# Performance work log

Hardware: AMD Instinct MI355X
Metric: run time of the kernel (lower is better)

Reference implementation:

```python
import jax, jax.numpy as jnp
import numpy as np

# ---- HashGridPlanesEncoder config (hybrid-k-planes) ----
NUM_LEVELS = 16
LEVEL_DIM = 2
BASE_RES = 16
DESIRED_RES = 2048
LOG2_HASHMAP = 19
D = 2  # grid_nd: each plane encoder is a 2D hash grid
N_PTS = 1048576
COO_COMBS = [(0, 1), (0, 2), (1, 2)]
HASH_PRIME_1 = 2654435761  # torch-ngp fast_hash prime for dim 1 (dim 0 prime is 1)


def _level_constants():
    # Mirrors torch-ngp GridEncoder offset/resolution computation.
    pls = 2.0 ** (np.log2(DESIRED_RES / BASE_RES) / (NUM_LEVELS - 1))
    max_params = 2 ** LOG2_HASHMAP
    scales, res, sizes, offs = [], [], [], [0]
    for l in range(NUM_LEVELS):
        s = BASE_RES * pls ** l - 1.0          # kernel: scale = exp2(l*S + H) - 1
        r = int(np.ceil(s)) + 1                # kernel: resolution = ceil(scale) + 1
        p = min(max_params, (r + 1) ** D)      # align_corners=False -> (res+1)^D
        p = int(np.ceil(p / 8) * 8)            # round up to multiple of 8
        scales.append(s); res.append(r); sizes.append(p); offs.append(offs[-1] + p)
    return (np.array(scales, np.float32), np.array(res, np.int64),
            np.array(sizes, np.int64), np.array(offs[:-1], np.int64), offs[-1])


SCALES, RES, SIZES, OFFSETS, TOTAL_PARAMS = _level_constants()
USE_HASH = ((RES + 1) ** D) > SIZES  # static per-level: dense linear index vs spatial hash


def _encode_plane(x2, table):
    """x2: [N,2] coords in [0,1]; table: [TOTAL_PARAMS, LEVEL_DIM]. Returns [N, L*C]."""
    n = x2.shape[0]
    scales = jnp.asarray(SCALES)
    pos = x2[:, None, :] * scales[None, :, None] + 0.5           # [N,L,2] (align_corners=False)
    pg_f = jnp.floor(pos)
    frac = pos - pg_f                                            # [N,L,2]
    pg = pg_f.astype(jnp.uint32)
    corners = jnp.array([[0, 0], [1, 0], [0, 1], [1, 1]], jnp.uint32)  # [4,2]
    cpos = pg[:, :, None, :] + corners[None, None]               # [N,L,4,2]
    cmask = corners.astype(bool)[None, None]                     # [1,1,4,2]
    w = jnp.where(cmask, frac[:, :, None, :], 1.0 - frac[:, :, None, :]).prod(-1)  # [N,L,4]
    stride1 = jnp.asarray((RES + 1).astype(np.uint32))           # [L]
    linear = cpos[..., 0] + cpos[..., 1] * stride1[None, :, None]
    hashed = cpos[..., 0] ^ (cpos[..., 1] * jnp.uint32(HASH_PRIME_1))  # uint32 wrap-around
    idx = jnp.where(jnp.asarray(USE_HASH)[None, :, None], hashed, linear)
    idx = idx % jnp.asarray(SIZES.astype(np.uint32))[None, :, None]
    idx = (idx + jnp.asarray(OFFSETS.astype(np.uint32))[None, :, None]).astype(jnp.int32)
    feats = table[idx]                                           # [N,L,4,C] gather
    out = (w[..., None] * feats).sum(axis=2)                     # [N,L,C] bilinear interp
    return out.reshape(n, NUM_LEVELS * LEVEL_DIM)


def setup_inputs() -> dict:
    key = jax.random.key(0)
    kp, k0, k1, k2 = jax.random.split(key, 4)
    pts = jax.random.uniform(kp, (N_PTS, 3), dtype=jnp.float32)  # coords (treated as in [-1,1] domain)
    std = 1e-4  # GridEncoder init: embeddings.uniform_(-1e-4, 1e-4)
    mk = lambda k: jax.random.uniform(k, (TOTAL_PARAMS, LEVEL_DIM), jnp.float32, -std, std)
    return {"pts": pts, "table_xy": mk(k0), "table_xz": mk(k1), "table_yz": mk(k2)}


def reference(pts, table_xy, table_xz, table_yz):
    # GridEncoder.forward normalizes inputs: (x + bound) / (2*bound), bound=1
    u = (pts + 1.0) * 0.5
    tables = (table_xy, table_xz, table_yz)
    out = _encode_plane(u[:, list(COO_COMBS[0])], tables[0])
    for comb, tab in zip(COO_COMBS[1:], tables[1:]):
        out = out + _encode_plane(u[:, list(comb)], tab)
    return out
```

## Files before the change

### kernel.cpp

```cpp
#include <hip/hip_runtime.h>
#include <hip/hip_fp16.h>
#include <cmath>

#define NLEV 16
#define HASH_START 12
#define HMASK ((1u << 19) - 1u)
#define HASH_PRIME 2654435761u
#define LDS_WORDS 14160

typedef float    f4 __attribute__((ext_vector_type(4)));
typedef unsigned u4 __attribute__((ext_vector_type(4)));

struct LvlC {
  float scale[NLEV];
  unsigned stride[NLEV];
  unsigned offset[NLEV];
};

__device__ __forceinline__ float2 h2f(unsigned u) {
  return __half22float2(__builtin_bit_cast(__half2, u));
}
__device__ __forceinline__ void nt_store4(float* p, float a, float b, float c, float d) {
  f4 v = {a, b, c, d};
  __builtin_nontemporal_store(v, reinterpret_cast<f4*>(p));
}

__global__ __launch_bounds__(256) void k_convert(
    const float2* __restrict__ t0, const float2* __restrict__ t1,
    const float2* __restrict__ t2, unsigned* __restrict__ dst, unsigned total)
{
  unsigned g = blockIdx.x * 256 + threadIdx.x;
  unsigned stp = gridDim.x * 256;
  unsigned tot3 = 3u * total;
  for (unsigned e = g; e < tot3; e += stp) {
    const float2* src; unsigned i = e;
    if (i < total)            { src = t0; }
    else if (i < 2u * total)  { src = t1; i -= total; }
    else                      { src = t2; i -= 2u * total; }
    float2 v = src[i];
    __half2 h = __floats2half2_rn(v.x, v.y);
    __builtin_nontemporal_store(__builtin_bit_cast(unsigned, h), dst + e);
  }
}

__global__ __launch_bounds__(256) void k_dense1011(
    const float* __restrict__ pts, const unsigned* __restrict__ tab,
    unsigned* __restrict__ s10, unsigned* __restrict__ s11,
    LvlC lc, unsigned total, int half)
{
  int t = blockIdx.x * 256 + threadIdx.x;
  if (t >= half) return;
  const int idx[2] = {t, t + half};

  float ua[2][3], ub[2][3];
#pragma unroll
  for (int k = 0; k < 2; ++k) {
    float u0 = (pts[3 * idx[k] + 0] + 1.f) * .5f;
    float u1 = (pts[3 * idx[k] + 1] + 1.f) * .5f;
    float u2 = (pts[3 * idx[k] + 2] + 1.f) * .5f;
    ua[k][0] = u0; ub[k][0] = u1;
    ua[k][1] = u0; ub[k][1] = u2;
    ua[k][2] = u1; ub[k][2] = u2;
  }

  uint2 g[2][2][3][2];
  float rx[2][2][3], ry[2][2][3];
#pragma unroll
  for (int k = 0; k < 2; ++k)
#pragma unroll
    for (int l = 0; l < 2; ++l) {
      const float sc = lc.scale[10 + l];
      const unsigned st = lc.stride[10 + l], o = lc.offset[10 + l];
#pragma unroll
      for (int p = 0; p < 3; ++p) {
        float px = ua[k][p] * sc + .5f, py = ub[k][p] * sc + .5f;
        float fx = floorf(px), fy = floorf(py);
        rx[k][l][p] = px - fx; ry[k][l][p] = py - fy;
        unsigned i00 = (unsigned)fx + (unsigned)fy * st + o;
        const unsigned* tp = tab + (size_t)p * total;
        g[k][l][p][0] = *reinterpret_cast<const uint2*>(tp + i00);
        g[k][l][p][1] = *reinterpret_cast<const uint2*>(tp + i00 + st);
      }
    }

#pragma unroll
  for (int k = 0; k < 2; ++k)
#pragma unroll
    for (int l = 0; l < 2; ++l) {
      float s0 = 0.f, s1 = 0.f;
#pragma unroll
      for (int p = 0; p < 3; ++p) {
        float x = rx[k][l][p], y = ry[k][l][p];
        float w00 = (1.f - x) * (1.f - y), w10 = x * (1.f - y);
        float w01 = (1.f - x) * y,          w11 = x * y;
        float2 f00 = h2f(g[k][l][p][0].x), f10 = h2f(g[k][l][p][0].y);
        float2 f01 = h2f(g[k][l][p][1].x), f11 = h2f(g[k][l][p][1].y);
        s0 += w00 * f00.x + w10 * f10.x + w01 * f01.x + w11 * f11.x;
        s1 += w00 * f00.y + w10 * f10.y + w01 * f01.y + w11 * f11.y;
      }
      unsigned hv = __builtin_bit_cast(unsigned, __floats2half2_rn(s0, s1));
      unsigned* sl = l ? s11 : s10;
      __builtin_nontemporal_store(hv, sl + idx[k]);
    }
}

__device__ __forceinline__ void hash_row(
    const unsigned* __restrict__ tp, unsigned x0, unsigned hy,
    unsigned& g0, unsigned& g1)
{
  unsigned a0 = (x0 ^ hy) & HMASK;
  if ((x0 & 1u) == 0u) {
    uint2 v = *reinterpret_cast<const uint2*>(tp + (a0 & ~1u));
    bool hi = (a0 & 1u) != 0u;
    g0 = hi ? v.y : v.x;
    g1 = hi ? v.x : v.y;
  } else {
    g0 = tp[a0];
    g1 = tp[((x0 + 1u) ^ hy) & HMASK];
  }
}

__global__ __launch_bounds__(256) void k_hash_lvl(
    const float* __restrict__ pts, const unsigned* __restrict__ tab,
    unsigned* __restrict__ slice, float sc, unsigned o, unsigned total, int half)
{
  int t = blockIdx.x * 256 + threadIdx.x;
  if (t >= half) return;
  const int idx[2] = {t, t + half};

  float ua[2][3], ub[2][3];
#pragma unroll
  for (int k = 0; k < 2; ++k) {
    float u0 = (pts[3 * idx[k] + 0] + 1.f) * .5f;
    float u1 = (pts[3 * idx[k] + 1] + 1.f) * .5f;
    float u2 = (pts[3 * idx[k] + 2] + 1.f) * .5f;
    ua[k][0] = u0; ub[k][0] = u1;
    ua[k][1] = u0; ub[k][1] = u2;
    ua[k][2] = u1; ub[k][2] = u2;
  }

  unsigned g[2][3][4];
  float rx[2][3], ry[2][3];
#pragma unroll
  for (int k = 0; k < 2; ++k)
#pragma unroll
    for (int p = 0; p < 3; ++p) {
      float px = ua[k][p] * sc + .5f, py = ub[k][p] * sc + .5f;
      float fx = floorf(px), fy = floorf(py);
      rx[k][p] = px - fx; ry[k][p] = py - fy;
      unsigned x0 = (unsigned)fx, y0 = (unsigned)fy;
      unsigned hy0 = y0 * HASH_PRIME, hy1 = hy0 + HASH_PRIME;
      const unsigned* tp = tab + (size_t)p * total + o;
      hash_row(tp, x0, hy0, g[k][p][0], g[k][p][1]);
      hash_row(tp, x0, hy1, g[k][p][2], g[k][p][3]);
    }

#pragma unroll
  for (int k = 0; k < 2; ++k) {
    float s0 = 0.f, s1 = 0.f;
#pragma unroll
    for (int p = 0; p < 3; ++p) {
      float x = rx[k][p], y = ry[k][p];
      float w00 = (1.f - x) * (1.f - y), w10 = x * (1.f - y);
      float w01 = (1.f - x) * y,          w11 = x * y;
      float2 f00 = h2f(g[k][p][0]), f10 = h2f(g[k][p][1]);
      float2 f01 = h2f(g[k][p][2]), f11 = h2f(g[k][p][3]);
      s0 += w00 * f00.x + w10 * f10.x + w01 * f01.x + w11 * f11.x;
      s1 += w00 * f00.y + w10 * f10.y + w01 * f01.y + w11 * f11.y;
    }
    __builtin_nontemporal_store(
        __builtin_bit_cast(unsigned, __floats2half2_rn(s0, s1)), slice + idx[k]);
  }
}

__global__ __launch_bounds__(512) void k_final(
    const float* __restrict__ pts, const unsigned* __restrict__ tab,
    const unsigned* __restrict__ slices,
    float* __restrict__ out, LvlC lc, unsigned total, int n)
{
  __shared__ unsigned lds[LDS_WORDS];
  int i = blockIdx.x * 512 + threadIdx.x;

  float u0 = (pts[3 * i + 0] + 1.f) * .5f;
  float u1 = (pts[3 * i + 1] + 1.f) * .5f;
  float u2 = (pts[3 * i + 2] + 1.f) * .5f;
  const float ua[3] = {u0, u0, u1}, ub[3] = {u1, u2, u2};

  float res[12];
#pragma unroll
  for (int j = 0; j < 12; ++j) res[j] = 0.f;

  for (int p = 0; p < 3; ++p) {
    if (p) __syncthreads();
    const u4* src = reinterpret_cast<const u4*>(tab + (size_t)p * total);
    for (unsigned e = threadIdx.x; e < LDS_WORDS / 4; e += 512)
      reinterpret_cast<u4*>(lds)[e] = src[e];
    __syncthreads();
#pragma unroll
    for (int l = 0; l < 6; ++l) {
      float px = ua[p] * lc.scale[l] + .5f, py = ub[p] * lc.scale[l] + .5f;
      float fx = floorf(px), fy = floorf(py);
      float x = px - fx, y = py - fy;
      unsigned st = lc.stride[l];
      unsigned i00 = (unsigned)fx + (unsigned)fy * st + lc.offset[l];
      float2 f00 = h2f(lds[i00]),      f10 = h2f(lds[i00 + 1]);
      float2 f01 = h2f(lds[i00 + st]), f11 = h2f(lds[i00 + st + 1]);
      float w00 = (1.f - x) * (1.f - y), w10 = x * (1.f - y);
      float w01 = (1.f - x) * y,          w11 = x * y;
      res[2 * l + 0] += w00 * f00.x + w10 * f10.x + w01 * f01.x + w11 * f11.x;
      res[2 * l + 1] += w00 * f00.y + w10 * f10.y + w01 * f01.y + w11 * f11.y;
    }
  }

  float res69[8];
#pragma unroll
  for (int grp = 0; grp < 2; ++grp) {
    uint2 g[2][3][2];
    float gx[2][3], gy[2][3];
#pragma unroll
    for (int h = 0; h < 2; ++h) {
      const int l = 6 + 2 * grp + h;
      const float sc = lc.scale[l];
      const unsigned st = lc.stride[l], o = lc.offset[l];
#pragma unroll
      for (int p = 0; p < 3; ++p) {
        float px = ua[p] * sc + .5f, py = ub[p] * sc + .5f;
        float fx = floorf(px), fy = floorf(py);
        gx[h][p] = px - fx; gy[h][p] = py - fy;
        unsigned i00 = (unsigned)fx + (unsigned)fy * st + o;
        const unsigned* tp = tab + (size_t)p * total;
        g[h][p][0] = *reinterpret_cast<const uint2*>(tp + i00);
        g[h][p][1] = *reinterpret_cast<const uint2*>(tp + i00 + st);
      }
    }
#pragma unroll
    for (int h = 0; h < 2; ++h) {
      float s0 = 0.f, s1 = 0.f;
#pragma unroll
      for (int p = 0; p < 3; ++p) {
        float x = gx[h][p], y = gy[h][p];
        float w00 = (1.f - x) * (1.f - y), w10 = x * (1.f - y);
        float w01 = (1.f - x) * y,          w11 = x * y;
        float2 f00 = h2f(g[h][p][0].x), f10 = h2f(g[h][p][0].y);
        float2 f01 = h2f(g[h][p][1].x), f11 = h2f(g[h][p][1].y);
        s0 += w00 * f00.x + w10 * f10.x + w01 * f01.x + w11 * f11.x;
        s1 += w00 * f00.y + w10 * f10.y + w01 * f01.y + w11 * f11.y;
      }
      res69[4 * grp + 2 * h + 0] = s0;
      res69[4 * grp + 2 * h + 1] = s1;
    }
  }

  unsigned sl[6];
#pragma unroll
  for (int j = 0; j < 6; ++j) sl[j] = slices[(size_t)j * n + i];

  float v[32];
#pragma unroll
  for (int j = 0; j < 12; ++j) v[j] = res[j];
#pragma unroll
  for (int j = 0; j < 8; ++j) v[12 + j] = res69[j];
#pragma unroll
  for (int j = 0; j < 6; ++j) {
    float2 f = h2f(sl[j]);
    v[20 + 2 * j] = f.x; v[20 + 2 * j + 1] = f.y;
  }
  float* orow = out + (size_t)i * 32;
#pragma unroll
  for (int j = 0; j < 8; ++j)
    nt_store4(orow + 4 * j, v[4 * j], v[4 * j + 1], v[4 * j + 2], v[4 * j + 3]);
}

__global__ __launch_bounds__(256) void k_fallback(
    const float* __restrict__ pts, const float2* __restrict__ txy,
    const float2* __restrict__ txz, const float2* __restrict__ tyz,
    float* __restrict__ out, LvlC lc, int n)
{
  int i = blockIdx.x * 256 + threadIdx.x;
  if (i >= n) return;
  float u0 = (pts[3 * i + 0] + 1.f) * .5f;
  float u1 = (pts[3 * i + 1] + 1.f) * .5f;
  float u2 = (pts[3 * i + 2] + 1.f) * .5f;
  const float ua[3] = {u0, u0, u1}, ub[3] = {u1, u2, u2};
  const float2* tabs[3] = {txy, txz, tyz};
  float acc[32];
#pragma unroll
  for (int j = 0; j < 32; ++j) acc[j] = 0.f;
#pragma unroll
  for (int l = 0; l < NLEV; ++l) {
    const float sc = lc.scale[l];
    const unsigned o = lc.offset[l], s = lc.stride[l];
#pragma unroll
    for (int p = 0; p < 3; ++p) {
      const float2* t = tabs[p];
      float px = ua[p] * sc + .5f, py = ub[p] * sc + .5f;
      float fx = floorf(px), fy = floorf(py);
      float rx = px - fx, ry = py - fy;
      unsigned x0 = (unsigned)fx, y0 = (unsigned)fy;
      float w00 = (1.f - rx) * (1.f - ry), w10 = rx * (1.f - ry);
      float w01 = (1.f - rx) * ry,          w11 = rx * ry;
      float2 f00, f10, f01, f11;
      if (l >= HASH_START) {
        unsigned hy0 = y0 * HASH_PRIME, hy1 = hy0 + HASH_PRIME;
        f00 = t[o + ((x0 ^ hy0) & HMASK)];
        f10 = t[o + (((x0 + 1u) ^ hy0) & HMASK)];
        f01 = t[o + ((x0 ^ hy1) & HMASK)];
        f11 = t[o + (((x0 + 1u) ^ hy1) & HMASK)];
      } else {
        unsigned i00 = x0 + y0 * s;
        float4 r0 = *reinterpret_cast<const float4*>(t + o + i00);
        float4 r1 = *reinterpret_cast<const float4*>(t + o + i00 + s);
        f00 = make_float2(r0.x, r0.y); f10 = make_float2(r0.z, r0.w);
        f01 = make_float2(r1.x, r1.y); f11 = make_float2(r1.z, r1.w);
      }
      acc[2 * l + 0] += w00 * f00.x + w10 * f10.x + w01 * f01.x + w11 * f11.x;
      acc[2 * l + 1] += w00 * f00.y + w10 * f10.y + w01 * f01.y + w11 * f11.y;
    }
  }
  float* orow = out + (size_t)i * 32;
#pragma unroll
  for (int j = 0; j < 8; ++j)
    nt_store4(orow + 4 * j, acc[4 * j], acc[4 * j + 1], acc[4 * j + 2], acc[4 * j + 3]);
}

static unsigned compute_levels(LvlC* lc)
{
  const double pls = std::pow(2.0, std::log2(2048.0 / 16.0) / 15.0);
  unsigned long long off = 0;
  for (int l = 0; l < NLEV; ++l) {
    double s = 16.0 * std::pow(pls, (double)l) - 1.0;
    lc->scale[l] = (float)s;
    long long r = (long long)std::ceil(s) + 1;
    long long dense = (r + 1) * (r + 1);
    long long sz = dense < (1LL << 19) ? dense : (1LL << 19);
    sz = ((sz + 7) / 8) * 8;
    lc->stride[l] = (unsigned)(r + 1);
    lc->offset[l] = (unsigned)off;
    off += (unsigned long long)sz;
  }
  return (unsigned)off;
}

extern "C" void kernel_launch(void* const* d_in, const int* in_sizes, int n_in,
                              void* d_out, int out_size, void* d_ws, size_t ws_size,
                              hipStream_t stream) {
  const float*  pts = (const float*)d_in[0];
  const float2* txy = (const float2*)d_in[1];
  const float2* txz = (const float2*)d_in[2];
  const float2* tyz = (const float2*)d_in[3];
  float* out = (float*)d_out;
  int n = in_sizes[0] / 3;

  LvlC lc;
  unsigned total = compute_levels(&lc);

  size_t tab_bytes = (size_t)3 * total * 4;
  size_t tab_al = (tab_bytes + 255) & ~(size_t)255;
  size_t need = tab_al + (size_t)6 * n * 4;

  bool ok = (n % 512 == 0) && (lc.offset[6] == LDS_WORDS) && (ws_size >= need);
  for (int l = HASH_START; l < NLEV; ++l) {
    unsigned sz = ((l + 1 < NLEV) ? lc.offset[l + 1] : total) - lc.offset[l];
    ok = ok && (sz == (1u << 19));
  }

  int block = 256;
  int grid = (n + block - 1) / block;
  if (!ok) {
    k_fallback<<<grid, block, 0, stream>>>(pts, txy, txz, tyz, out, lc, n);
    return;
  }

  unsigned* tab16 = (unsigned*)d_ws;
  unsigned* slices = (unsigned*)((char*)d_ws + tab_al);

  int half = n / 2;
  int gridh = half / block;

  k_convert<<<2048, 256, 0, stream>>>(txy, txz, tyz, tab16, total);
  k_dense1011<<<gridh, block, 0, stream>>>(pts, tab16, slices, slices + (size_t)n,
                                           lc, total, half);
  for (int l = HASH_START; l < NLEV; ++l)
    k_hash_lvl<<<gridh, block, 0, stream>>>(pts, tab16, slices + (size_t)(l - 10) * n,
                                            lc.scale[l], lc.offset[l], total, half);
  k_final<<<n / 512, 512, 0, stream>>>(pts, tab16, slices, out, lc, total, n);
}
```

Before: 366.3 us.

## Halve LDS footprint by staging level 5 separately; hoist slice loads; use plain stores

The LDS table for k_final shrinks from 14160 words to 7432: levels 0-4 are staged first, then level 5 is loaded separately into the same buffer, which adds an extra load and syncs per plane. The smaller LDS use is meant to let more workgroups share a CU and hide latency better. The slice loads move to the top of the kernel so their global latency overlaps the compute. Output stores change from nontemporal to ordinary float4 stores, which may alter cache behaviour on the large output write.

```diff
diff --git a/kernel.cpp b/kernel.cpp
--- a/kernel.cpp
+++ b/kernel.cpp
@@ -6,7 +6,8 @@
 #define HASH_START 12
 #define HMASK ((1u << 19) - 1u)
 #define HASH_PRIME 2654435761u
-#define LDS_WORDS 14160
+#define LDSA_WORDS 7432
+#define LDS5_WORDS 6728
 
 typedef float    f4 __attribute__((ext_vector_type(4)));
 typedef unsigned u4 __attribute__((ext_vector_type(4)));
@@ -178,8 +179,12 @@
     const unsigned* __restrict__ slices,
     float* __restrict__ out, LvlC lc, unsigned total, int n)
 {
-  __shared__ unsigned lds[LDS_WORDS];
+  __shared__ unsigned lds[LDSA_WORDS];
   int i = blockIdx.x * 512 + threadIdx.x;
+
+  unsigned sl[6];
+#pragma unroll
+  for (int j = 0; j < 6; ++j) sl[j] = slices[(size_t)j * n + i];
 
   float u0 = (pts[3 * i + 0] + 1.f) * .5f;
   float u1 = (pts[3 * i + 1] + 1.f) * .5f;
@@ -191,13 +196,13 @@
   for (int j = 0; j < 12; ++j) res[j] = 0.f;
 
   for (int p = 0; p < 3; ++p) {
+    const unsigned* tp = tab + (size_t)p * total;
     if (p) __syncthreads();
-    const u4* src = reinterpret_cast<const u4*>(tab + (size_t)p * total);
-    for (unsigned e = threadIdx.x; e < LDS_WORDS / 4; e += 512)
-      reinterpret_cast<u4*>(lds)[e] = src[e];
+    for (unsigned e = threadIdx.x; e < LDSA_WORDS / 4; e += 512)
+      reinterpret_cast<u4*>(lds)[e] = reinterpret_cast<const u4*>(tp)[e];
     __syncthreads();
 #pragma unroll
-    for (int l = 0; l < 6; ++l) {
+    for (int l = 0; l < 5; ++l) {
       float px = ua[p] * lc.scale[l] + .5f, py = ub[p] * lc.scale[l] + .5f;
       float fx = floorf(px), fy = floorf(py);
       float x = px - fx, y = py - fy;
@@ -210,6 +215,24 @@
       res[2 * l + 0] += w00 * f00.x + w10 * f10.x + w01 * f01.x + w11 * f11.x;
       res[2 * l + 1] += w00 * f00.y + w10 * f10.y + w01 * f01.y + w11 * f11.y;
     }
+    __syncthreads();
+    {
+      const u4* src5 = reinterpret_cast<const u4*>(tp + lc.offset[5]);
+      for (unsigned e = threadIdx.x; e < LDS5_WORDS / 4; e += 512)
+        reinterpret_cast<u4*>(lds)[e] = src5[e];
+      __syncthreads();
+      float px = ua[p] * lc.scale[5] + .5f, py = ub[p] * lc.scale[5] + .5f;
+      float fx = floorf(px), fy = floorf(py);
+      float x = px - fx, y = py - fy;
+      unsigned st = lc.stride[5];
+      unsigned i00 = (unsigned)fx + (unsigned)fy * st;
+      float2 f00 = h2f(lds[i00]),      f10 = h2f(lds[i00 + 1]);
+      float2 f01 = h2f(lds[i00 + st]), f11 = h2f(lds[i00 + st + 1]);
+      float w00 = (1.f - x) * (1.f - y), w10 = x * (1.f - y);
+      float w01 = (1.f - x) * y,          w11 = x * y;
+      res[10] += w00 * f00.x + w10 * f10.x + w01 * f01.x + w11 * f11.x;
+      res[11] += w00 * f00.y + w10 * f10.y + w01 * f01.y + w11 * f11.y;
+    }
   }
 
   float res69[8];
@@ -251,10 +274,6 @@
     }
   }
 
-  unsigned sl[6];
-#pragma unroll
-  for (int j = 0; j < 6; ++j) sl[j] = slices[(size_t)j * n + i];
-
   float v[32];
 #pragma unroll
   for (int j = 0; j < 12; ++j) v[j] = res[j];
@@ -265,10 +284,10 @@
     float2 f = h2f(sl[j]);
     v[20 + 2 * j] = f.x; v[20 + 2 * j + 1] = f.y;
   }
-  float* orow = out + (size_t)i * 32;
+  float4* o4 = (float4*)(out + (size_t)i * 32);
 #pragma unroll
   for (int j = 0; j < 8; ++j)
-    nt_store4(orow + 4 * j, v[4 * j], v[4 * j + 1], v[4 * j + 2], v[4 * j + 3]);
+    o4[j] = make_float4(v[4 * j], v[4 * j + 1], v[4 * j + 2], v[4 * j + 3]);
 }
 
 __global__ __launch_bounds__(256) void k_fallback(
@@ -317,10 +336,10 @@
       acc[2 * l + 1] += w00 * f00.y + w10 * f10.y + w01 * f01.y + w11 * f11.y;
     }
   }
-  float* orow = out + (size_t)i * 32;
+  float4* o4 = (float4*)(out + (size_t)i * 32);
 #pragma unroll
   for (int j = 0; j < 8; ++j)
-    nt_store4(orow + 4 * j, acc[4 * j], acc[4 * j + 1], acc[4 * j + 2], acc[4 * j + 3]);
+    o4[j] = make_float4(acc[4 * j], acc[4 * j + 1], acc[4 * j + 2], acc[4 * j + 3]);
 }
 
 static unsigned compute_levels(LvlC* lc)
@@ -358,7 +377,8 @@
   size_t tab_al = (tab_bytes + 255) & ~(size_t)255;
   size_t need = tab_al + (size_t)6 * n * 4;
 
-  bool ok = (n % 512 == 0) && (lc.offset[6] == LDS_WORDS) && (ws_size >= need);
+  bool ok = (n % 512 == 0) && (lc.offset[5] == LDSA_WORDS) &&
+            (lc.offset[6] - lc.offset[5] == LDS5_WORDS) && (ws_size >= need);
   for (int l = HASH_START; l < NLEV; ++l) {
     unsigned sz = ((l + 1 < NLEV) ? lc.offset[l + 1] : total) - lc.offset[l];
     ok = ok && (sz == (1u << 19));
```

After: 374.7 us. 1.02x slower.

## Move levels 6-9 out of final kernel into separate dense-pair slice passes

Applied to the files above, without the earlier changes.

Generalizes the dense level-pair kernel to take per-level constants and, when workspace allows, runs it for level pairs 6-7, 8-9 and 10-11, writing ten fp16 slices. The final kernel then only does the LDS levels 0-5 and unpacks slices, with the slice loads issued at kernel start. Output stores change from nontemporal to plain float4 stores. This shortens the final kernel's register-heavy gather phase at the cost of two extra launches and more slice traffic through memory.

```diff
diff --git a/kernel.cpp b/kernel.cpp
--- a/kernel.cpp
+++ b/kernel.cpp
@@ -19,10 +19,6 @@
 
 __device__ __forceinline__ float2 h2f(unsigned u) {
   return __half22float2(__builtin_bit_cast(__half2, u));
-}
-__device__ __forceinline__ void nt_store4(float* p, float a, float b, float c, float d) {
-  f4 v = {a, b, c, d};
-  __builtin_nontemporal_store(v, reinterpret_cast<f4*>(p));
 }
 
 __global__ __launch_bounds__(256) void k_convert(
@@ -43,10 +39,12 @@
   }
 }
 
-__global__ __launch_bounds__(256) void k_dense1011(
+__global__ __launch_bounds__(256) void k_dense_pair(
     const float* __restrict__ pts, const unsigned* __restrict__ tab,
-    unsigned* __restrict__ s10, unsigned* __restrict__ s11,
-    LvlC lc, unsigned total, int half)
+    unsigned* __restrict__ sA, unsigned* __restrict__ sB,
+    float scA, unsigned stA, unsigned oA,
+    float scB, unsigned stB, unsigned oB,
+    unsigned total, int half)
 {
   int t = blockIdx.x * 256 + threadIdx.x;
   if (t >= half) return;
@@ -62,26 +60,25 @@
     ua[k][1] = u0; ub[k][1] = u2;
     ua[k][2] = u1; ub[k][2] = u2;
   }
+  const float sc[2] = {scA, scB};
+  const unsigned st[2] = {stA, stB}, o[2] = {oA, oB};
 
   uint2 g[2][2][3][2];
   float rx[2][2][3], ry[2][2][3];
 #pragma unroll
   for (int k = 0; k < 2; ++k)
 #pragma unroll
-    for (int l = 0; l < 2; ++l) {
-      const float sc = lc.scale[10 + l];
-      const unsigned st = lc.stride[10 + l], o = lc.offset[10 + l];
+    for (int l = 0; l < 2; ++l)
 #pragma unroll
       for (int p = 0; p < 3; ++p) {
-        float px = ua[k][p] * sc + .5f, py = ub[k][p] * sc + .5f;
+        float px = ua[k][p] * sc[l] + .5f, py = ub[k][p] * sc[l] + .5f;
         float fx = floorf(px), fy = floorf(py);
         rx[k][l][p] = px - fx; ry[k][l][p] = py - fy;
-        unsigned i00 = (unsigned)fx + (unsigned)fy * st + o;
+        unsigned i00 = (unsigned)fx + (unsigned)fy * st[l] + o[l];
         const unsigned* tp = tab + (size_t)p * total;
         g[k][l][p][0] = *reinterpret_cast<const uint2*>(tp + i00);
-        g[k][l][p][1] = *reinterpret_cast<const uint2*>(tp + i00 + st);
+        g[k][l][p][1] = *reinterpret_cast<const uint2*>(tp + i00 + st[l]);
       }
-    }
 
 #pragma unroll
   for (int k = 0; k < 2; ++k)
@@ -99,8 +96,7 @@
         s1 += w00 * f00.y + w10 * f10.y + w01 * f01.y + w11 * f11.y;
       }
       unsigned hv = __builtin_bit_cast(unsigned, __floats2half2_rn(s0, s1));
-      unsigned* sl = l ? s11 : s10;
-      __builtin_nontemporal_store(hv, sl + idx[k]);
+      __builtin_nontemporal_store(hv, (l ? sB : sA) + idx[k]);
     }
 }
 
@@ -173,6 +169,7 @@
   }
 }
 
+template <bool DO69>
 __global__ __launch_bounds__(512) void k_final(
     const float* __restrict__ pts, const unsigned* __restrict__ tab,
     const unsigned* __restrict__ slices,
@@ -180,6 +177,11 @@
 {
   __shared__ unsigned lds[LDS_WORDS];
   int i = blockIdx.x * 512 + threadIdx.x;
+
+  const int NS = DO69 ? 6 : 10;
+  unsigned sl[DO69 ? 6 : 10];
+#pragma unroll
+  for (int j = 0; j < NS; ++j) sl[j] = slices[(size_t)j * n + i];
 
   float u0 = (pts[3 * i + 0] + 1.f) * .5f;
   float u1 = (pts[3 * i + 1] + 1.f) * .5f;
@@ -212,63 +214,65 @@
     }
   }
 
-  float res69[8];
-#pragma unroll
-  for (int grp = 0; grp < 2; ++grp) {
-    uint2 g[2][3][2];
-    float gx[2][3], gy[2][3];
-#pragma unroll
-    for (int h = 0; h < 2; ++h) {
-      const int l = 6 + 2 * grp + h;
-      const float sc = lc.scale[l];
-      const unsigned st = lc.stride[l], o = lc.offset[l];
-#pragma unroll
-      for (int p = 0; p < 3; ++p) {
-        float px = ua[p] * sc + .5f, py = ub[p] * sc + .5f;
-        float fx = floorf(px), fy = floorf(py);
-        gx[h][p] = px - fx; gy[h][p] = py - fy;
-        unsigned i00 = (unsigned)fx + (unsigned)fy * st + o;
-        const unsigned* tp = tab + (size_t)p * total;
-        g[h][p][0] = *reinterpret_cast<const uint2*>(tp + i00);
-        g[h][p][1] = *reinterpret_cast<const uint2*>(tp + i00 + st);
+  float v[32];
+#pragma unroll
+  for (int j = 0; j < 12; ++j) v[j] = res[j];
+
+  if (DO69) {
+#pragma unroll
+    for (int grp = 0; grp < 2; ++grp) {
+      uint2 g[2][3][2];
+      float gx[2][3], gy[2][3];
+#pragma unroll
+      for (int h = 0; h < 2; ++h) {
+        const int l = 6 + 2 * grp + h;
+        const float sc = lc.scale[l];
+        const unsigned st = lc.stride[l], o = lc.offset[l];
+#pragma unroll
+        for (int p = 0; p < 3; ++p) {
+          float px = ua[p] * sc + .5f, py = ub[p] * sc + .5f;
+          float fx = floorf(px), fy = floorf(py);
+          gx[h][p] = px - fx; gy[h][p] = py - fy;
+          unsigned i00 = (unsigned)fx + (unsigned)fy * st + o;
+          const unsigned* tp = tab + (size_t)p * total;
+          g[h][p][0] = *reinterpret_cast<const uint2*>(tp + i00);
+          g[h][p][1] = *reinterpret_cast<const uint2*>(tp + i00 + st);
+        }
       }
-    }
-#pragma unroll
-    for (int h = 0; h < 2; ++h) {
-      float s0 = 0.f, s1 = 0.f;
-#pragma unroll
-      for (int p = 0; p < 3; ++p) {
-        float x = gx[h][p], y = gy[h][p];
-        float w00 = (1.f - x) * (1.f - y), w10 = x * (1.f - y);
-        float w01 = (1.f - x) * y,          w11 = x * y;
-        float2 f00 = h2f(g[h][p][0].x), f10 = h2f(g[h][p][0].y);
-        float2 f01 = h2f(g[h][p][1].x), f11 = h2f(g[h][p][1].y);
-        s0 += w00 * f00.x + w10 * f10.x + w01 * f01.x + w11 * f11.x;
-        s1 += w00 * f00.y + w10 * f10.y + w01 * f01.y + w11 * f11.y;
+#pragma unroll
+      for (int h = 0; h < 2; ++h) {
+        float s0 = 0.f, s1 = 0.f;
+#pragma unroll
+        for (int p = 0; p < 3; ++p) {
+          float x = gx[h][p], y = gy[h][p];
+          float w00 = (1.f - x) * (1.f - y), w10 = x * (1.f - y);
+          float w01 = (1.f - x) * y,          w11 = x * y;
+          float2 f00 = h2f(g[h][p][0].x), f10 = h2f(g[h][p][0].y);
+          float2 f01 = h2f(g[h][p][1].x), f11 = h2f(g[h][p][1].y);
+          s0 += w00 * f00.x + w10 * f10.x + w01 * f01.x + w11 * f11.x;
+          s1 += w00 * f00.y + w10 * f10.y + w01 * f01.y + w11 * f11.y;
+        }
+        v[12 + 4 * grp + 2 * h + 0] = s0;
+        v[12 + 4 * grp + 2 * h + 1] = s1;
       }
-      res69[4 * grp + 2 * h + 0] = s0;
-      res69[4 * grp + 2 * h + 1] = s1;
-    }
-  }
-
-  unsigned sl[6];
-#pragma unroll
-  for (int j = 0; j < 6; ++j) sl[j] = slices[(size_t)j * n + i];
-
-  float v[32];
-#pragma unroll
-  for (int j = 0; j < 12; ++j) v[j] = res[j];
-#pragma unroll
-  for (int j = 0; j < 8; ++j) v[12 + j] = res69[j];
-#pragma unroll
-  for (int j = 0; j < 6; ++j) {
-    float2 f = h2f(sl[j]);
-    v[20 + 2 * j] = f.x; v[20 + 2 * j + 1] = f.y;
-  }
-  float* orow = out + (size_t)i * 32;
+    }
+#pragma unroll
+    for (int j = 0; j < 6; ++j) {
+      float2 f = h2f(sl[j]);
+      v[20 + 2 * j] = f.x; v[20 + 2 * j + 1] = f.y;
+    }
+  } else {
+#pragma unroll
+    for (int j = 0; j < 10; ++j) {
+      float2 f = h2f(sl[j]);
+      v[12 + 2 * j] = f.x; v[12 + 2 * j + 1] = f.y;
+    }
+  }
+
+  float4* o4 = (float4*)(out + (size_t)i * 32);
 #pragma unroll
   for (int j = 0; j < 8; ++j)
-    nt_store4(orow + 4 * j, v[4 * j], v[4 * j + 1], v[4 * j + 2], v[4 * j + 3]);
+    o4[j] = make_float4(v[4 * j], v[4 * j + 1], v[4 * j + 2], v[4 * j + 3]);
 }
 
 __global__ __launch_bounds__(256) void k_fallback(
@@ -317,10 +321,10 @@
       acc[2 * l + 1] += w00 * f00.y + w10 * f10.y + w01 * f01.y + w11 * f11.y;
     }
   }
-  float* orow = out + (size_t)i * 32;
+  float4* o4 = (float4*)(out + (size_t)i * 32);
 #pragma unroll
   for (int j = 0; j < 8; ++j)
-    nt_store4(orow + 4 * j, acc[4 * j], acc[4 * j + 1], acc[4 * j + 2], acc[4 * j + 3]);
+    o4[j] = make_float4(acc[4 * j], acc[4 * j + 1], acc[4 * j + 2], acc[4 * j + 3]);
 }
 
 static unsigned compute_levels(LvlC* lc)
@@ -356,32 +360,50 @@
 
   size_t tab_bytes = (size_t)3 * total * 4;
   size_t tab_al = (tab_bytes + 255) & ~(size_t)255;
-  size_t need = tab_al + (size_t)6 * n * 4;
-
-  bool ok = (n % 512 == 0) && (lc.offset[6] == LDS_WORDS) && (ws_size >= need);
+  size_t need10 = tab_al + (size_t)10 * n * 4;
+  size_t need6  = tab_al + (size_t)6 * n * 4;
+
+  bool base_ok = (n % 512 == 0) && (lc.offset[6] == LDS_WORDS);
   for (int l = HASH_START; l < NLEV; ++l) {
     unsigned sz = ((l + 1 < NLEV) ? lc.offset[l + 1] : total) - lc.offset[l];
-    ok = ok && (sz == (1u << 19));
+    base_ok = base_ok && (sz == (1u << 19));
   }
 
   int block = 256;
   int grid = (n + block - 1) / block;
-  if (!ok) {
+  if (!base_ok || ws_size < need6) {
     k_fallback<<<grid, block, 0, stream>>>(pts, txy, txz, tyz, out, lc, n);
     return;
   }
 
   unsigned* tab16 = (unsigned*)d_ws;
   unsigned* slices = (unsigned*)((char*)d_ws + tab_al);
-
   int half = n / 2;
   int gridh = half / block;
 
   k_convert<<<2048, 256, 0, stream>>>(txy, txz, tyz, tab16, total);
-  k_dense1011<<<gridh, block, 0, stream>>>(pts, tab16, slices, slices + (size_t)n,
-                                           lc, total, half);
-  for (int l = HASH_START; l < NLEV; ++l)
-    k_hash_lvl<<<gridh, block, 0, stream>>>(pts, tab16, slices + (size_t)(l - 10) * n,
-                                            lc.scale[l], lc.offset[l], total, half);
-  k_final<<<n / 512, 512, 0, stream>>>(pts, tab16, slices, out, lc, total, n);
-}
+
+  if (ws_size >= need10) {
+    for (int grp = 0; grp < 3; ++grp) {
+      int lA = 6 + 2 * grp, lB = lA + 1;
+      k_dense_pair<<<gridh, block, 0, stream>>>(
+          pts, tab16,
+          slices + (size_t)(lA - 6) * n, slices + (size_t)(lB - 6) * n,
+          lc.scale[lA], lc.stride[lA], lc.offset[lA],
+          lc.scale[lB], lc.stride[lB], lc.offset[lB], total, half);
+    }
+    for (int l = HASH_START; l < NLEV; ++l)
+      k_hash_lvl<<<gridh, block, 0, stream>>>(pts, tab16, slices + (size_t)(l - 6) * n,
+                                              lc.scale[l], lc.offset[l], total, half);
+    k_final<false><<<n / 512, 512, 0, stream>>>(pts, tab16, slices, out, lc, total, n);
+  } else {
+    k_dense_pair<<<gridh, block, 0, stream>>>(
+        pts, tab16, slices, slices + (size_t)n,
+        lc.scale[10], lc.stride[10], lc.offset[10],
+        lc.scale[11], lc.stride[11], lc.offset[11], total, half);
+    for (int l = HASH_START; l < NLEV; ++l)
+      k_hash_lvl<<<gridh, block, 0, stream>>>(pts, tab16, slices + (size_t)(l - 10) * n,
+                                              lc.scale[l], lc.offset[l], total, half);
+    k_final<true><<<n / 512, 512, 0, stream>>>(pts, tab16, slices, out, lc, total, n);
+  }
+}
```

New measurement: 357.1 us. 2.5% less time.

## Fuse dense levels 10-11 into final kernel and overlap gathers with LDS fill

Applied to the files above, without the earlier changes.

Drops the separate k_dense1011 launch and computes levels 6-11 inside k_final. Each level pair's global gathers are issued while that plane's LDS table is being filled, so global latency overlaps the LDS copy and barrier. This removes one launch and the write/read round trip of two fp16 slice arrays, and shrinks the workspace. Output stores switch from nontemporal to plain float4 stores. The cost is more work and register pressure per thread in k_final, which may lower occupancy.

```diff
diff --git a/kernel.cpp b/kernel.cpp
--- a/kernel.cpp
+++ b/kernel.cpp
@@ -19,10 +19,6 @@
 
 __device__ __forceinline__ float2 h2f(unsigned u) {
   return __half22float2(__builtin_bit_cast(__half2, u));
-}
-__device__ __forceinline__ void nt_store4(float* p, float a, float b, float c, float d) {
-  f4 v = {a, b, c, d};
-  __builtin_nontemporal_store(v, reinterpret_cast<f4*>(p));
 }
 
 __global__ __launch_bounds__(256) void k_convert(
@@ -43,67 +39,6 @@
   }
 }
 
-__global__ __launch_bounds__(256) void k_dense1011(
-    const float* __restrict__ pts, const unsigned* __restrict__ tab,
-    unsigned* __restrict__ s10, unsigned* __restrict__ s11,
-    LvlC lc, unsigned total, int half)
-{
-  int t = blockIdx.x * 256 + threadIdx.x;
-  if (t >= half) return;
-  const int idx[2] = {t, t + half};
-
-  float ua[2][3], ub[2][3];
-#pragma unroll
-  for (int k = 0; k < 2; ++k) {
-    float u0 = (pts[3 * idx[k] + 0] + 1.f) * .5f;
-    float u1 = (pts[3 * idx[k] + 1] + 1.f) * .5f;
-    float u2 = (pts[3 * idx[k] + 2] + 1.f) * .5f;
-    ua[k][0] = u0; ub[k][0] = u1;
-    ua[k][1] = u0; ub[k][1] = u2;
-    ua[k][2] = u1; ub[k][2] = u2;
-  }
-
-  uint2 g[2][2][3][2];
-  float rx[2][2][3], ry[2][2][3];
-#pragma unroll
-  for (int k = 0; k < 2; ++k)
-#pragma unroll
-    for (int l = 0; l < 2; ++l) {
-      const float sc = lc.scale[10 + l];
-      const unsigned st = lc.stride[10 + l], o = lc.offset[10 + l];
-#pragma unroll
-      for (int p = 0; p < 3; ++p) {
-        float px = ua[k][p] * sc + .5f, py = ub[k][p] * sc + .5f;
-        float fx = floorf(px), fy = floorf(py);
-        rx[k][l][p] = px - fx; ry[k][l][p] = py - fy;
-        unsigned i00 = (unsigned)fx + (unsigned)fy * st + o;
-        const unsigned* tp = tab + (size_t)p * total;
-        g[k][l][p][0] = *reinterpret_cast<const uint2*>(tp + i00);
-        g[k][l][p][1] = *reinterpret_cast<const uint2*>(tp + i00 + st);
-      }
-    }
-
-#pragma unroll
-  for (int k = 0; k < 2; ++k)
-#pragma unroll
-    for (int l = 0; l < 2; ++l) {
-      float s0 = 0.f, s1 = 0.f;
-#pragma unroll
-      for (int p = 0; p < 3; ++p) {
-        float x = rx[k][l][p], y = ry[k][l][p];
-        float w00 = (1.f - x) * (1.f - y), w10 = x * (1.f - y);
-        float w01 = (1.f - x) * y,          w11 = x * y;
-        float2 f00 = h2f(g[k][l][p][0].x), f10 = h2f(g[k][l][p][0].y);
-        float2 f01 = h2f(g[k][l][p][1].x), f11 = h2f(g[k][l][p][1].y);
-        s0 += w00 * f00.x + w10 * f10.x + w01 * f01.x + w11 * f11.x;
-        s1 += w00 * f00.y + w10 * f10.y + w01 * f01.y + w11 * f11.y;
-      }
-      unsigned hv = __builtin_bit_cast(unsigned, __floats2half2_rn(s0, s1));
-      unsigned* sl = l ? s11 : s10;
-      __builtin_nontemporal_store(hv, sl + idx[k]);
-    }
-}
-
 __device__ __forceinline__ void hash_row(
     const unsigned* __restrict__ tp, unsigned x0, unsigned hy,
     unsigned& g0, unsigned& g1)
@@ -186,23 +121,44 @@
   float u2 = (pts[3 * i + 2] + 1.f) * .5f;
   const float ua[3] = {u0, u0, u1}, ub[3] = {u1, u2, u2};
 
-  float res[12];
+  float res[24];
 #pragma unroll
   for (int j = 0; j < 12; ++j) res[j] = 0.f;
 
+  uint2 g[2][3][2];
+  float gx[2][3], gy[2][3];
+
+#pragma unroll 1
   for (int p = 0; p < 3; ++p) {
     if (p) __syncthreads();
     const u4* src = reinterpret_cast<const u4*>(tab + (size_t)p * total);
     for (unsigned e = threadIdx.x; e < LDS_WORDS / 4; e += 512)
       reinterpret_cast<u4*>(lds)[e] = src[e];
+#pragma unroll
+    for (int h = 0; h < 2; ++h) {
+      const int l = 6 + 2 * p + h;
+      const float sc = lc.scale[l];
+      const unsigned st = lc.stride[l], o = lc.offset[l];
+#pragma unroll
+      for (int q = 0; q < 3; ++q) {
+        float px = ua[q] * sc + .5f, py = ub[q] * sc + .5f;
+        float fx = floorf(px), fy = floorf(py);
+        gx[h][q] = px - fx; gy[h][q] = py - fy;
+        unsigned i00 = (unsigned)fx + (unsigned)fy * st + o;
+        const unsigned* tp = tab + (size_t)q * total;
+        g[h][q][0] = *reinterpret_cast<const uint2*>(tp + i00);
+        g[h][q][1] = *reinterpret_cast<const uint2*>(tp + i00 + st);
+      }
+    }
     __syncthreads();
 #pragma unroll
     for (int l = 0; l < 6; ++l) {
-      float px = ua[p] * lc.scale[l] + .5f, py = ub[p] * lc.scale[l] + .5f;
+      const float sc = lc.scale[l];
+      const unsigned st = lc.stride[l], o = lc.offset[l];
+      float px = ua[p] * sc + .5f, py = ub[p] * sc + .5f;
       float fx = floorf(px), fy = floorf(py);
       float x = px - fx, y = py - fy;
-      unsigned st = lc.stride[l];
-      unsigned i00 = (unsigned)fx + (unsigned)fy * st + lc.offset[l];
+      unsigned i00 = (unsigned)fx + (unsigned)fy * st + o;
       float2 f00 = h2f(lds[i00]),      f10 = h2f(lds[i00 + 1]);
       float2 f01 = h2f(lds[i00 + st]), f11 = h2f(lds[i00 + st + 1]);
       float w00 = (1.f - x) * (1.f - y), w10 = x * (1.f - y);
@@ -210,65 +166,40 @@
       res[2 * l + 0] += w00 * f00.x + w10 * f10.x + w01 * f01.x + w11 * f11.x;
       res[2 * l + 1] += w00 * f00.y + w10 * f10.y + w01 * f01.y + w11 * f11.y;
     }
-  }
-
-  float res69[8];
-#pragma unroll
-  for (int grp = 0; grp < 2; ++grp) {
-    uint2 g[2][3][2];
-    float gx[2][3], gy[2][3];
-#pragma unroll
-    for (int h = 0; h < 2; ++h) {
-      const int l = 6 + 2 * grp + h;
-      const float sc = lc.scale[l];
-      const unsigned st = lc.stride[l], o = lc.offset[l];
-#pragma unroll
-      for (int p = 0; p < 3; ++p) {
-        float px = ua[p] * sc + .5f, py = ub[p] * sc + .5f;
-        float fx = floorf(px), fy = floorf(py);
-        gx[h][p] = px - fx; gy[h][p] = py - fy;
-        unsigned i00 = (unsigned)fx + (unsigned)fy * st + o;
-        const unsigned* tp = tab + (size_t)p * total;
-        g[h][p][0] = *reinterpret_cast<const uint2*>(tp + i00);
-        g[h][p][1] = *reinterpret_cast<const uint2*>(tp + i00 + st);
-      }
-    }
 #pragma unroll
     for (int h = 0; h < 2; ++h) {
       float s0 = 0.f, s1 = 0.f;
 #pragma unroll
-      for (int p = 0; p < 3; ++p) {
-        float x = gx[h][p], y = gy[h][p];
+      for (int q = 0; q < 3; ++q) {
+        float x = gx[h][q], y = gy[h][q];
         float w00 = (1.f - x) * (1.f - y), w10 = x * (1.f - y);
         float w01 = (1.f - x) * y,          w11 = x * y;
-        float2 f00 = h2f(g[h][p][0].x), f10 = h2f(g[h][p][0].y);
-        float2 f01 = h2f(g[h][p][1].x), f11 = h2f(g[h][p][1].y);
+        float2 f00 = h2f(g[h][q][0].x), f10 = h2f(g[h][q][0].y);
+        float2 f01 = h2f(g[h][q][1].x), f11 = h2f(g[h][q][1].y);
         s0 += w00 * f00.x + w10 * f10.x + w01 * f01.x + w11 * f11.x;
         s1 += w00 * f00.y + w10 * f10.y + w01 * f01.y + w11 * f11.y;
       }
-      res69[4 * grp + 2 * h + 0] = s0;
-      res69[4 * grp + 2 * h + 1] = s1;
-    }
-  }
-
-  unsigned sl[6];
-#pragma unroll
-  for (int j = 0; j < 6; ++j) sl[j] = slices[(size_t)j * n + i];
+      res[12 + 4 * p + 2 * h + 0] = s0;
+      res[12 + 4 * p + 2 * h + 1] = s1;
+    }
+  }
+
+  unsigned sl[4];
+#pragma unroll
+  for (int j = 0; j < 4; ++j) sl[j] = slices[(size_t)j * n + i];
 
   float v[32];
 #pragma unroll
-  for (int j = 0; j < 12; ++j) v[j] = res[j];
-#pragma unroll
-  for (int j = 0; j < 8; ++j) v[12 + j] = res69[j];
-#pragma unroll
-  for (int j = 0; j < 6; ++j) {
+  for (int j = 0; j < 24; ++j) v[j] = res[j];
+#pragma unroll
+  for (int j = 0; j < 4; ++j) {
     float2 f = h2f(sl[j]);
-    v[20 + 2 * j] = f.x; v[20 + 2 * j + 1] = f.y;
-  }
-  float* orow = out + (size_t)i * 32;
+    v[24 + 2 * j] = f.x; v[24 + 2 * j + 1] = f.y;
+  }
+  float4* o4 = (float4*)(out + (size_t)i * 32);
 #pragma unroll
   for (int j = 0; j < 8; ++j)
-    nt_store4(orow + 4 * j, v[4 * j], v[4 * j + 1], v[4 * j + 2], v[4 * j + 3]);
+    o4[j] = make_float4(v[4 * j], v[4 * j + 1], v[4 * j + 2], v[4 * j + 3]);
 }
 
 __global__ __launch_bounds__(256) void k_fallback(
@@ -317,10 +248,10 @@
       acc[2 * l + 1] += w00 * f00.y + w10 * f10.y + w01 * f01.y + w11 * f11.y;
     }
   }
-  float* orow = out + (size_t)i * 32;
+  float4* o4 = (float4*)(out + (size_t)i * 32);
 #pragma unroll
   for (int j = 0; j < 8; ++j)
-    nt_store4(orow + 4 * j, acc[4 * j], acc[4 * j + 1], acc[4 * j + 2], acc[4 * j + 3]);
+    o4[j] = make_float4(acc[4 * j], acc[4 * j + 1], acc[4 * j + 2], acc[4 * j + 3]);
 }
 
 static unsigned compute_levels(LvlC* lc)
@@ -356,7 +287,7 @@
 
   size_t tab_bytes = (size_t)3 * total * 4;
   size_t tab_al = (tab_bytes + 255) & ~(size_t)255;
-  size_t need = tab_al + (size_t)6 * n * 4;
+  size_t need = tab_al + (size_t)4 * n * 4;
 
   bool ok = (n % 512 == 0) && (lc.offset[6] == LDS_WORDS) && (ws_size >= need);
   for (int l = HASH_START; l < NLEV; ++l) {
@@ -378,10 +309,8 @@
   int gridh = half / block;
 
   k_convert<<<2048, 256, 0, stream>>>(txy, txz, tyz, tab16, total);
-  k_dense1011<<<gridh, block, 0, stream>>>(pts, tab16, slices, slices + (size_t)n,
-                                           lc, total, half);
   for (int l = HASH_START; l < NLEV; ++l)
-    k_hash_lvl<<<gridh, block, 0, stream>>>(pts, tab16, slices + (size_t)(l - 10) * n,
+    k_hash_lvl<<<gridh, block, 0, stream>>>(pts, tab16, slices + (size_t)(l - 12) * n,
                                             lc.scale[l], lc.offset[l], total, half);
   k_final<<<n / 512, 512, 0, stream>>>(pts, tab16, slices, out, lc, total, n);
 }
```

Result: faster. 321.0 us (median of 2 runs) (-12.4%).
